# Optimization experiments

Measured on AMD Instinct MI355X. Metric: run time of the kernel, lower is better.

## Reference

```python
import jax, jax.numpy as jnp
import numpy as np

N = 50000      # nodes per node type
E = 800000     # edges per meta-step (avg degree 16)
DIN = 16       # input feature dim (all node types)
DMSG = 16      # dim_message per meta-step
F = 16         # edge feature dim
DOUT = 32      # dim_out of final linear


def setup_inputs() -> dict:
    key = jax.random.key(0)
    ks = jax.random.split(key, 17)
    s = 0.1  # param scale
    return {
        "x_indivi": jax.random.normal(ks[0], (N, DIN), jnp.float32),
        "x_src_a": jax.random.normal(ks[1], (N, DIN), jnp.float32),
        "x_src_b": jax.random.normal(ks[2], (N, DIN), jnp.float32),
        "edge_index_a": jax.random.randint(ks[3], (2, E), 0, N),
        "edge_index_b": jax.random.randint(ks[4], (2, E), 0, N),
        "edge_attr_a": jax.random.normal(ks[5], (E, F), jnp.float32),
        "edge_attr_b": jax.random.normal(ks[6], (E, F), jnp.float32),
        # message_function of NNConv: Linear(F, DIN*DMSG), stored as [F, DIN, DMSG]
        "w_msg_a": jax.random.normal(ks[7], (F, DIN, DMSG), jnp.float32) * s,
        "b_msg_a": jax.random.normal(ks[8], (DIN, DMSG), jnp.float32) * s,
        "root_a": jax.random.normal(ks[9], (DIN, DMSG), jnp.float32) * s,
        "bias_a": jax.random.normal(ks[10], (DMSG,), jnp.float32) * s,
        "w_msg_b": jax.random.normal(ks[11], (F, DIN, DMSG), jnp.float32) * s,
        "b_msg_b": jax.random.normal(ks[12], (DIN, DMSG), jnp.float32) * s,
        "root_b": jax.random.normal(ks[13], (DIN, DMSG), jnp.float32) * s,
        "bias_b": jax.random.normal(ks[14], (DMSG,), jnp.float32) * s,
        # final linear: Linear(2*DMSG, DOUT), stored as [2*DMSG, DOUT]
        "w_lin": jax.random.normal(ks[15], (2 * DMSG, DOUT), jnp.float32) * s,
        "b_lin": jax.random.normal(ks[16], (DOUT,), jnp.float32) * s,
    }


def _nnconv(x_src, x_dst, edge_index, edge_attr, w_msg, b_msg, root, bias):
    """PyG NNConv with sum aggregation.
    W_e = edge_attr @ w_msg + b_msg  (per-edge [DIN, DMSG] weight matrix)
    msg_e = x_src[src_e] @ W_e ; out = segment_sum(msg) + x_dst @ root + bias
    """
    src, dst = edge_index[0], edge_index[1]
    xj = x_src[src]  # [E, DIN] gather
    # fused per-edge bmm: einsum contracts without keeping W_e longer than needed
    msg = jnp.einsum('ef,fio,ei->eo', edge_attr, w_msg, xj) + xj @ b_msg  # [E, DMSG]
    agg = jax.ops.segment_sum(msg, dst, num_segments=x_dst.shape[0])  # scatter-add
    return agg + x_dst @ root + bias


def reference(x_indivi, x_src_a, x_src_b, edge_index_a, edge_index_b,
              edge_attr_a, edge_attr_b,
              w_msg_a, b_msg_a, root_a, bias_a,
              w_msg_b, b_msg_b, root_b, bias_b,
              w_lin, b_lin):
    msg_a = jax.nn.sigmoid(_nnconv(x_src_a, x_indivi, edge_index_a, edge_attr_a,
                                   w_msg_a, b_msg_a, root_a, bias_a))
    msg_b = jax.nn.sigmoid(_nnconv(x_src_b, x_indivi, edge_index_b, edge_attr_b,
                                   w_msg_b, b_msg_b, root_b, bias_b))
    msg_cat = jnp.concatenate([msg_a, msg_b], axis=1)  # [N, 2*DMSG]
    return jax.nn.sigmoid(msg_cat @ w_lin + b_lin)     # [N, DOUT]
```

## Files before the change

kernel.cpp:

```cpp
#include <hip/hip_runtime.h>
#include <hip/hip_bf16.h>
#include <stdint.h>


#define NN 50000
#define EE 800000

typedef __attribute__((ext_vector_type(8))) short short8;
typedef __attribute__((ext_vector_type(4))) float f32x4;

union U8 { short8 v; unsigned int u[4]; };

__device__ __forceinline__ unsigned short f2bf_rne(float f) {
    union { float fl; unsigned int i; } v; v.fl = f;
    unsigned int x = v.i;
    x += 0x7FFFu + ((x >> 16) & 1u);
    return (unsigned short)(x >> 16);
}

__device__ __forceinline__ unsigned int pack2bf(float a, float b) {
    __hip_bfloat162 h = __float22bfloat162_rn(float2{a, b});
    union { __hip_bfloat162 h2; unsigned int u; } c; c.h2 = h;
    return c.u;
}

__global__ void prep_w(const float* __restrict__ w_msg, const float* __restrict__ b_msg,
                       unsigned short* __restrict__ wfrag) {
    for (int idx = threadIdx.x; idx < 9 * 64 * 8; idx += 256) {
        int j = idx & 7;
        int lane = (idx >> 3) & 63;
        int t = idx >> 9;
        int k = 32 * t + (lane >> 4) * 8 + j;
        int n = lane & 15;
        int f = k >> 4, i = k & 15;
        float v = (f < 16) ? w_msg[f * 256 + i * 16 + n]
                           : (f == 16 ? b_msg[i * 16 + n] : 0.f);
        wfrag[idx] = f2bf_rne(v);
    }
}

__global__ __launch_bounds__(256) void edge_mfma(
    const int* __restrict__ eidx, const float* __restrict__ attr,
    const float* __restrict__ x, const unsigned short* __restrict__ wfrag,
    float* __restrict__ agg)
{
    int lane = threadIdx.x & 63;
    int m = lane & 15, quad = lane >> 4;
    int q2 = quad >> 1, qb = quad & 1;
    int wave = (blockIdx.x * 256 + (int)threadIdx.x) >> 6;
    int nwaves = (gridDim.x * 256) >> 6;

    short8 bfr[9];
    #pragma unroll
    for (int t = 0; t < 9; ++t)
        bfr[t] = ((const short8*)wfrag)[t * 64 + lane];

    for (int g = wave; g < EE / 16; g += nwaves) {
        int ebase = g * 16;
        int src = eidx[ebase + m];
        int dstr[4];
        #pragma unroll
        for (int r = 0; r < 4; ++r)
            dstr[r] = eidx[EE + ebase + quad * 4 + r];

        const float4* xr = (const float4*)(x + (size_t)src * 16);
        float4 x0 = xr[qb * 2];
        float4 x1 = xr[qb * 2 + 1];
        float xh[8] = {x0.x, x0.y, x0.z, x0.w, x1.x, x1.y, x1.z, x1.w};

        const float* ar = attr + (size_t)(ebase + m) * 16;
        float ah[8];
        #pragma unroll
        for (int t = 0; t < 8; ++t) ah[t] = ar[2 * t + q2];

        f32x4 acc = {0.f, 0.f, 0.f, 0.f};
        #pragma unroll
        for (int t = 0; t < 8; ++t) {
            U8 a;
            #pragma unroll
            for (int jj = 0; jj < 4; ++jj)
                a.u[jj] = pack2bf(ah[t] * xh[2 * jj], ah[t] * xh[2 * jj + 1]);
            acc = __builtin_amdgcn_mfma_f32_16x16x32_bf16(a.v, bfr[t], acc, 0, 0, 0);
        }
        U8 a8;
        #pragma unroll
        for (int jj = 0; jj < 4; ++jj)
            a8.u[jj] = (q2 == 0) ? pack2bf(xh[2 * jj], xh[2 * jj + 1]) : 0u;
        acc = __builtin_amdgcn_mfma_f32_16x16x32_bf16(a8.v, bfr[8], acc, 0, 0, 0);

        #pragma unroll
        for (int r = 0; r < 4; ++r)
            atomicAdd(&agg[dstr[r] * 16 + m], acc[r]);
    }
}

__global__ __launch_bounds__(256) void finalize(
    const float* __restrict__ xind,
    const float* __restrict__ agg_a, const float* __restrict__ agg_b,
    const float* __restrict__ root_a, const float* __restrict__ bias_a,
    const float* __restrict__ root_b, const float* __restrict__ bias_b,
    const float* __restrict__ w_lin, const float* __restrict__ b_lin,
    float* __restrict__ out)
{
    int tid = threadIdx.x;
    int n = blockIdx.x * 8 + (tid >> 5);
    if (n >= NN) return;
    int d = tid & 31;
    int lane = tid & 63;
    int gb32 = lane & ~31;

    float xv = xind[n * 16 + (d & 15)];

    int j = d & 15;
    const float* root = (d < 16) ? root_a : root_b;
    const float* bias = (d < 16) ? bias_a : bias_b;
    const float* agg  = (d < 16) ? agg_a  : agg_b;

    float acc = agg[n * 16 + j] + bias[j];
    #pragma unroll
    for (int i = 0; i < 16; ++i) {
        float xiv = __shfl(xv, gb32 + i);
        acc += xiv * root[i * 16 + j];
    }
    float h = 1.f / (1.f + __expf(-acc));

    float acc2 = b_lin[d];
    #pragma unroll
    for (int jj = 0; jj < 32; ++jj) {
        float hj = __shfl(h, gb32 + jj);
        acc2 += hj * w_lin[jj * 32 + d];
    }
    out[(size_t)n * 32 + d] = 1.f / (1.f + __expf(-acc2));
}

extern "C" void kernel_launch(void* const* d_in, const int* in_sizes, int n_in,
                              void* d_out, int out_size, void* d_ws, size_t ws_size,
                              hipStream_t stream) {
    (void)in_sizes; (void)n_in; (void)out_size; (void)ws_size;
    const float* x_indivi = (const float*)d_in[0];
    const float* x_src_a  = (const float*)d_in[1];
    const float* x_src_b  = (const float*)d_in[2];
    const int*   ei_a     = (const int*)d_in[3];
    const int*   ei_b     = (const int*)d_in[4];
    const float* ea_a     = (const float*)d_in[5];
    const float* ea_b     = (const float*)d_in[6];
    const float* w_msg_a  = (const float*)d_in[7];
    const float* b_msg_a  = (const float*)d_in[8];
    const float* root_a   = (const float*)d_in[9];
    const float* bias_a   = (const float*)d_in[10];
    const float* w_msg_b  = (const float*)d_in[11];
    const float* b_msg_b  = (const float*)d_in[12];
    const float* root_b   = (const float*)d_in[13];
    const float* bias_b   = (const float*)d_in[14];
    const float* w_lin    = (const float*)d_in[15];
    const float* b_lin    = (const float*)d_in[16];
    float* out = (float*)d_out;

    char* ws = (char*)d_ws;
    size_t off = 0;
    unsigned short* wf_a = (unsigned short*)(ws + off); off += 9 * 64 * 8 * 2;
    unsigned short* wf_b = (unsigned short*)(ws + off); off += 9 * 64 * 8 * 2;
    float* agg_a = (float*)(ws + off); off += (size_t)NN * 16 * 4;
    float* agg_b = (float*)(ws + off); off += (size_t)NN * 16 * 4;

    hipMemsetAsync(agg_a, 0, (size_t)NN * 16 * 4 * 2, stream);
    prep_w<<<1, 256, 0, stream>>>(w_msg_a, b_msg_a, wf_a);
    prep_w<<<1, 256, 0, stream>>>(w_msg_b, b_msg_b, wf_b);

    edge_mfma<<<1024, 256, 0, stream>>>(ei_a, ea_a, x_src_a, wf_a, agg_a);
    edge_mfma<<<1024, 256, 0, stream>>>(ei_b, ea_b, x_src_b, wf_b, agg_b);

    finalize<<<(NN + 7) / 8, 256, 0, stream>>>(
        x_indivi, agg_a, agg_b, root_a, bias_a, root_b, bias_b, w_lin, b_lin, out);
}
```

Before: 304.3 us.

## Privatize scatter-add buffers per XCD and use workgroup-scope atomics

Each edge kernel reads its XCC id from a hardware register and scatter-adds into a private copy of the aggregation buffer for that die. This lets the atomics be issued at workgroup scope instead of device scope, which is meant to cut the cost of cross-die coherent fp32 atomics. The finalize kernel then sums the eight copies, and the memset now clears 8x more memory. Also adds nontemporal loads for edge data, merges the two prep_w launches into one, and doubles the edge grid. The extra memset and reduction traffic, and relying on workgroup scope being correct because all blocks on one XCD share its L2, are the costs and risks.

```diff
diff --git a/kernel.cpp b/kernel.cpp
--- a/kernel.cpp
+++ b/kernel.cpp
@@ -5,6 +5,7 @@
 
 #define NN 50000
 #define EE 800000
+#define AGGSZ ((size_t)NN * 16)
 
 typedef __attribute__((ext_vector_type(8))) short short8;
 typedef __attribute__((ext_vector_type(4))) float f32x4;
@@ -24,8 +25,13 @@
     return c.u;
 }
 
-__global__ void prep_w(const float* __restrict__ w_msg, const float* __restrict__ b_msg,
-                       unsigned short* __restrict__ wfrag) {
+__global__ void prep_w(const float* __restrict__ w_msg_a, const float* __restrict__ b_msg_a,
+                       unsigned short* __restrict__ wf_a,
+                       const float* __restrict__ w_msg_b, const float* __restrict__ b_msg_b,
+                       unsigned short* __restrict__ wf_b) {
+    const float* w_msg = blockIdx.x ? w_msg_b : w_msg_a;
+    const float* b_msg = blockIdx.x ? b_msg_b : b_msg_a;
+    unsigned short* wfrag = blockIdx.x ? wf_b : wf_a;
     for (int idx = threadIdx.x; idx < 9 * 64 * 8; idx += 256) {
         int j = idx & 7;
         int lane = (idx >> 3) & 63;
@@ -42,13 +48,16 @@
 __global__ __launch_bounds__(256) void edge_mfma(
     const int* __restrict__ eidx, const float* __restrict__ attr,
     const float* __restrict__ x, const unsigned short* __restrict__ wfrag,
-    float* __restrict__ agg)
+    float* __restrict__ aggc)
 {
+    int xcc = (int)(__builtin_amdgcn_s_getreg((3 << 11) | 20) & 7u);
+    float* __restrict__ agg = aggc + (size_t)xcc * AGGSZ;
+
     int lane = threadIdx.x & 63;
     int m = lane & 15, quad = lane >> 4;
     int q2 = quad >> 1, qb = quad & 1;
     int wave = (blockIdx.x * 256 + (int)threadIdx.x) >> 6;
-    int nwaves = (gridDim.x * 256) >> 6;
+    int nwaves = gridDim.x * 4;
 
     short8 bfr[9];
     #pragma unroll
@@ -57,21 +66,21 @@
 
     for (int g = wave; g < EE / 16; g += nwaves) {
         int ebase = g * 16;
-        int src = eidx[ebase + m];
+        int src = __builtin_nontemporal_load(&eidx[ebase + m]);
         int dstr[4];
         #pragma unroll
         for (int r = 0; r < 4; ++r)
-            dstr[r] = eidx[EE + ebase + quad * 4 + r];
+            dstr[r] = __builtin_nontemporal_load(&eidx[EE + ebase + quad * 4 + r]);
 
-        const float4* xr = (const float4*)(x + (size_t)src * 16);
-        float4 x0 = xr[qb * 2];
-        float4 x1 = xr[qb * 2 + 1];
+        const f32x4* xr = (const f32x4*)(x + (size_t)src * 16);
+        f32x4 x0 = __builtin_nontemporal_load(xr + qb * 2);
+        f32x4 x1 = __builtin_nontemporal_load(xr + qb * 2 + 1);
         float xh[8] = {x0.x, x0.y, x0.z, x0.w, x1.x, x1.y, x1.z, x1.w};
 
         const float* ar = attr + (size_t)(ebase + m) * 16;
         float ah[8];
         #pragma unroll
-        for (int t = 0; t < 8; ++t) ah[t] = ar[2 * t + q2];
+        for (int t = 0; t < 8; ++t) ah[t] = __builtin_nontemporal_load(&ar[2 * t + q2]);
 
         f32x4 acc = {0.f, 0.f, 0.f, 0.f};
         #pragma unroll
@@ -90,13 +99,14 @@
 
         #pragma unroll
         for (int r = 0; r < 4; ++r)
-            atomicAdd(&agg[dstr[r] * 16 + m], acc[r]);
+            __hip_atomic_fetch_add(&agg[(size_t)dstr[r] * 16 + m], acc[r],
+                                   __ATOMIC_RELAXED, __HIP_MEMORY_SCOPE_WORKGROUP);
     }
 }
 
 __global__ __launch_bounds__(256) void finalize(
     const float* __restrict__ xind,
-    const float* __restrict__ agg_a, const float* __restrict__ agg_b,
+    const float* __restrict__ aggc_a, const float* __restrict__ aggc_b,
     const float* __restrict__ root_a, const float* __restrict__ bias_a,
     const float* __restrict__ root_b, const float* __restrict__ bias_b,
     const float* __restrict__ w_lin, const float* __restrict__ b_lin,
@@ -114,9 +124,12 @@
     int j = d & 15;
     const float* root = (d < 16) ? root_a : root_b;
     const float* bias = (d < 16) ? bias_a : bias_b;
-    const float* agg  = (d < 16) ? agg_a  : agg_b;
+    const float* aggc = (d < 16) ? aggc_a : aggc_b;
 
-    float acc = agg[n * 16 + j] + bias[j];
+    float acc = bias[j];
+    #pragma unroll
+    for (int c = 0; c < 8; ++c)
+        acc += aggc[(size_t)c * AGGSZ + n * 16 + j];
     #pragma unroll
     for (int i = 0; i < 16; ++i) {
         float xiv = __shfl(xv, gb32 + i);
@@ -160,16 +173,15 @@
     size_t off = 0;
     unsigned short* wf_a = (unsigned short*)(ws + off); off += 9 * 64 * 8 * 2;
     unsigned short* wf_b = (unsigned short*)(ws + off); off += 9 * 64 * 8 * 2;
-    float* agg_a = (float*)(ws + off); off += (size_t)NN * 16 * 4;
-    float* agg_b = (float*)(ws + off); off += (size_t)NN * 16 * 4;
+    float* aggc_a = (float*)(ws + off); off += 8 * AGGSZ * 4;
+    float* aggc_b = (float*)(ws + off); off += 8 * AGGSZ * 4;
 
-    hipMemsetAsync(agg_a, 0, (size_t)NN * 16 * 4 * 2, stream);
-    prep_w<<<1, 256, 0, stream>>>(w_msg_a, b_msg_a, wf_a);
-    prep_w<<<1, 256, 0, stream>>>(w_msg_b, b_msg_b, wf_b);
+    (void)hipMemsetAsync(aggc_a, 0, 16 * AGGSZ * 4, stream);
+    prep_w<<<2, 256, 0, stream>>>(w_msg_a, b_msg_a, wf_a, w_msg_b, b_msg_b, wf_b);
 
-    edge_mfma<<<1024, 256, 0, stream>>>(ei_a, ea_a, x_src_a, wf_a, agg_a);
-    edge_mfma<<<1024, 256, 0, stream>>>(ei_b, ea_b, x_src_b, wf_b, agg_b);
+    edge_mfma<<<2048, 256, 0, stream>>>(ei_a, ea_a, x_src_a, wf_a, aggc_a);
+    edge_mfma<<<2048, 256, 0, stream>>>(ei_b, ea_b, x_src_b, wf_b, aggc_b);
 
     finalize<<<(NN + 7) / 8, 256, 0, stream>>>(
-        x_indivi, agg_a, agg_b, root_a, bias_a, root_b, bias_b, w_lin, b_lin, out);
+        x_indivi, aggc_a, aggc_b, root_a, bias_a, root_b, bias_b, w_lin, b_lin, out);
 }
```

New measurement: 332.7 us. 9.3% more time.
